# Performance work log

Measured on AMD Instinct MI355X. Metric: run time of the kernel, lower is better.

The kernel has to match this reference:

```python
import jax, jax.numpy as jnp
import numpy as np


def setup_inputs() -> dict:
    key = jax.random.key(0)
    k1, k2 = jax.random.split(key)
    B, T, D = 16, 512, 384
    MAX_LEN = 4096
    x = jax.random.normal(k1, (B, T, D), dtype=jnp.float32)
    durations = jax.random.randint(k2, (B, T), 0, 8, dtype=jnp.int64)
    return {"x": x, "durations": durations, "max_len": MAX_LEN}


def reference(x, durations, max_len):
    # x: (B, T, D), durations: (B, T) int
    B, T, D = x.shape
    cum = jnp.cumsum(durations, axis=1)          # (B, T) exclusive-of-nothing cumulative ends
    mel_len = cum[:, -1]                         # (B,) actual (uncapped) frame lengths
    frames = jnp.arange(max_len)                 # (F,)
    # phoneme index owning each output frame: searchsorted on cumulative ends
    idx = jax.vmap(lambda c: jnp.searchsorted(c, frames, side='right'))(cum)  # (B, F)
    idx = jnp.clip(idx, 0, T - 1)
    out = jnp.take_along_axis(x, idx[:, :, None], axis=1)  # (B, F, D)
    # zero-pad frames beyond each item's length (and beyond max_len truncation)
    valid = frames[None, :] < jnp.minimum(mel_len, max_len)[:, None]  # (B, F)
    out = out * valid[:, :, None].astype(out.dtype)
    return out, mel_len
```

## Files before the change

### kernel.cpp

```cpp
#include <hip/hip_runtime.h>


#define B_ 16
#define T_ 512
#define D_ 384
#define MAXLEN_ 4096
#define ROWV4_ (D_ / 4)
#define OUT_ELEMS_ (B_ * MAXLEN_ * D_)

__global__ __launch_bounds__(T_) void lr_scan_kernel(const int* __restrict__ dur,
                                                     const int* __restrict__ max_len_p,
                                                     int* __restrict__ ws_idx,
                                                     float* __restrict__ mel_out) {
    __shared__ int s[T_];
    const int b = blockIdx.x;
    const int t = threadIdx.x;
    const int max_len = max_len_p[0];

    const int d = dur[b * T_ + t];
    s[t] = d;
    __syncthreads();

    #pragma unroll
    for (int off = 1; off < T_; off <<= 1) {
        const int add = (t >= off) ? s[t - off] : 0;
        __syncthreads();
        s[t] += add;
        __syncthreads();
    }
    const int cum = s[t];
    const int start = cum - d;
    const int mel = s[T_ - 1];

    int* wb = ws_idx + b * MAXLEN_;
    for (int j = t; j < MAXLEN_; j += T_) wb[j] = -1;
    __syncthreads();

    for (int j = 0; j < d; ++j) {
        const int f = start + j;
        if (f < max_len && f < MAXLEN_) wb[f] = t;
    }

    if (t == 0) mel_out[b] = (float)mel;
}

__global__ __launch_bounds__(256) void lr_gather_kernel(const float4* __restrict__ x,
                                                        const int* __restrict__ ws_idx,
                                                        float4* __restrict__ out) {
    const int g = blockIdx.x * 256 + threadIdx.x;
    const int row = g / ROWV4_;
    const int col = g - row * ROWV4_;
    const int idx = ws_idx[row];
    float4 v;
    if (idx >= 0) {
        const int b = row >> 12;
        v = x[(b * T_ + idx) * ROWV4_ + col];
    } else {
        v = make_float4(0.f, 0.f, 0.f, 0.f);
    }
    out[g] = v;
}

extern "C" void kernel_launch(void* const* d_in, const int* in_sizes, int n_in,
                              void* d_out, int out_size, void* d_ws, size_t ws_size,
                              hipStream_t stream) {
    const float* x = (const float*)d_in[0];
    const int* dur = (const int*)d_in[1];
    const int* max_len_p = (const int*)d_in[2];

    float* out = (float*)d_out;
    float* mel_out = out + OUT_ELEMS_;
    int* ws_idx = (int*)d_ws;

    lr_scan_kernel<<<B_, T_, 0, stream>>>(dur, max_len_p, ws_idx, mel_out);

    const int total_v4 = OUT_ELEMS_ / 4;
    lr_gather_kernel<<<total_v4 / 256, 256, 0, stream>>>(
        (const float4*)x, ws_idx, (float4*)out);
}
```

Baseline: 125.1 us.

## Replace frame-index scatter with per-block binary search over cumulative durations

```diff
diff --git a/kernel.cpp b/kernel.cpp
--- a/kernel.cpp
+++ b/kernel.cpp
@@ -7,56 +7,64 @@
 #define MAXLEN_ 4096
 #define ROWV4_ (D_ / 4)
 #define OUT_ELEMS_ (B_ * MAXLEN_ * D_)
+#define BLOCKS_PER_BATCH_ ((MAXLEN_ * ROWV4_) / 256)
 
 __global__ __launch_bounds__(T_) void lr_scan_kernel(const int* __restrict__ dur,
-                                                     const int* __restrict__ max_len_p,
-                                                     int* __restrict__ ws_idx,
+                                                     int* __restrict__ cum_ws,
                                                      float* __restrict__ mel_out) {
-    __shared__ int s[T_];
-    const int b = blockIdx.x;
-    const int t = threadIdx.x;
-    const int max_len = max_len_p[0];
-
-    const int d = dur[b * T_ + t];
-    s[t] = d;
+    const int b = blockIdx.x, t = threadIdx.x;
+    const int lane = t & 63, w = t >> 6;
+    int v = dur[b * T_ + t];
+    #pragma unroll
+    for (int off = 1; off < 64; off <<= 1) {
+        int n = __shfl_up(v, off);
+        if (lane >= off) v += n;
+    }
+    __shared__ int wsum[8];
+    if (lane == 63) wsum[w] = v;
     __syncthreads();
-
-    #pragma unroll
-    for (int off = 1; off < T_; off <<= 1) {
-        const int add = (t >= off) ? s[t - off] : 0;
-        __syncthreads();
-        s[t] += add;
-        __syncthreads();
+    if (t < 8) {
+        int u = wsum[t];
+        #pragma unroll
+        for (int off = 1; off < 8; off <<= 1) {
+            int n = __shfl_up(u, off);
+            if (t >= off) u += n;
+        }
+        wsum[t] = u;
     }
-    const int cum = s[t];
-    const int start = cum - d;
-    const int mel = s[T_ - 1];
-
-    int* wb = ws_idx + b * MAXLEN_;
-    for (int j = t; j < MAXLEN_; j += T_) wb[j] = -1;
     __syncthreads();
-
-    for (int j = 0; j < d; ++j) {
-        const int f = start + j;
-        if (f < max_len && f < MAXLEN_) wb[f] = t;
-    }
-
-    if (t == 0) mel_out[b] = (float)mel;
+    const int cum = v + (w > 0 ? wsum[w - 1] : 0);
+    cum_ws[b * T_ + t] = cum;
+    if (t == T_ - 1) mel_out[b] = (float)cum;
 }
 
 __global__ __launch_bounds__(256) void lr_gather_kernel(const float4* __restrict__ x,
-                                                        const int* __restrict__ ws_idx,
+                                                        const int* __restrict__ cum_ws,
+                                                        const int* __restrict__ max_len_p,
                                                         float4* __restrict__ out) {
-    const int g = blockIdx.x * 256 + threadIdx.x;
+    __shared__ int s[T_];
+    const int t = threadIdx.x;
+    const int b = blockIdx.x / BLOCKS_PER_BATCH_;
+    const int* cb = cum_ws + b * T_;
+    s[t] = cb[t];
+    s[t + 256] = cb[t + 256];
+    __syncthreads();
+
+    const int g = blockIdx.x * 256 + t;
     const int row = g / ROWV4_;
     const int col = g - row * ROWV4_;
-    const int idx = ws_idx[row];
-    float4 v;
-    if (idx >= 0) {
-        const int b = row >> 12;
+    const int f = row & (MAXLEN_ - 1);
+    const int mel = s[T_ - 1];
+    const int max_len = max_len_p[0];
+
+    float4 v = make_float4(0.f, 0.f, 0.f, 0.f);
+    if (f < mel && f < max_len) {
+        int idx = 0;
+        #pragma unroll
+        for (int step = 256; step > 0; step >>= 1)
+            if (s[idx + step - 1] <= f) idx += step;
+        if (idx > T_ - 1) idx = T_ - 1;
         v = x[(b * T_ + idx) * ROWV4_ + col];
-    } else {
-        v = make_float4(0.f, 0.f, 0.f, 0.f);
     }
     out[g] = v;
 }
@@ -70,11 +78,11 @@
 
     float* out = (float*)d_out;
     float* mel_out = out + OUT_ELEMS_;
-    int* ws_idx = (int*)d_ws;
+    int* cum_ws = (int*)d_ws;
 
-    lr_scan_kernel<<<B_, T_, 0, stream>>>(dur, max_len_p, ws_idx, mel_out);
+    lr_scan_kernel<<<B_, T_, 0, stream>>>(dur, cum_ws, mel_out);
 
     const int total_v4 = OUT_ELEMS_ / 4;
     lr_gather_kernel<<<total_v4 / 256, 256, 0, stream>>>(
-        (const float4*)x, ws_idx, (float4*)out);
+        (const float4*)x, cum_ws, max_len_p, (float4*)out);
 }
```

Result: faster. 122.3 us (median of 2 runs) (-2.3%).
